# Performance work log

Hardware: AMD Instinct MI355X
Metric: run time of the kernel (lower is better)

The kernel has to match this reference:

```python
import jax, jax.numpy as jnp
import numpy as np

H, C = 5, 128          # heads, hidden_channels
NUM_GRAPHS = 500
N_NODES, N_EDGES = 20000, 320000


def gat_layer(x, edge_attr, src, dst, W, We, a_src, a_dst, a_edge, b):
    """PyG GATConv with edge_dim, add_self_loops=True, fill_value='mean', concat heads."""
    N = x.shape[0]
    ed = edge_attr.dtype
    # self-loop edge_attr = scatter-mean of incoming edge_attr per target node
    deg = jax.ops.segment_sum(jnp.ones((dst.shape[0],), ed), dst, num_segments=N)
    loop_attr = jax.ops.segment_sum(edge_attr, dst, num_segments=N) / jnp.maximum(deg, 1.0)[:, None]
    loop = jnp.arange(N, dtype=src.dtype)
    s = jnp.concatenate([src, loop])
    d = jnp.concatenate([dst, loop])
    ea = jnp.concatenate([edge_attr, loop_attr], axis=0)
    h = (x @ W).reshape(N, H, C)            # [N,H,C]
    e = (ea @ We).reshape(-1, H, C)         # [E2,H,C]
    a_l = (h * a_src).sum(-1)               # [N,H]
    a_r = (h * a_dst).sum(-1)               # [N,H]
    a_e = (e * a_edge).sum(-1)              # [E2,H]
    alpha = jax.nn.leaky_relu(a_l[s] + a_r[d] + a_e, 0.2)
    # segment softmax over destination neighborhoods
    amax = jax.ops.segment_max(alpha, d, num_segments=N)
    ex = jnp.exp(alpha - amax[d])
    denom = jax.ops.segment_sum(ex, d, num_segments=N)
    att = ex / (denom[d] + 1e-16)           # [E2,H]
    msg = h[s] * att[..., None]             # [E2,H,C]
    out = jax.ops.segment_sum(msg, d, num_segments=N).reshape(N, H * C)
    return out + b


def setup_inputs() -> dict:
    key = jax.random.key(0)
    ks = jax.random.split(key, 24)
    p = lambda k, sh: (jax.random.normal(k, sh, dtype=jnp.float32) * 0.05)
    inp = {
        "x": jax.random.normal(ks[0], (N_NODES, 43), dtype=jnp.float32),
        "edge_attr": jax.random.normal(ks[1], (N_EDGES, 10), dtype=jnp.float32),
        "W1": p(ks[2], (43, H * C)),   "We1": p(ks[3], (10, H * C)),
        "asrc1": p(ks[4], (H, C)), "adst1": p(ks[5], (H, C)), "aedge1": p(ks[6], (H, C)),
        "b1": jnp.zeros((H * C,), jnp.float32),
        "W2": p(ks[7], (H * C, H * C)), "We2": p(ks[8], (10, H * C)),
        "asrc2": p(ks[9], (H, C)), "adst2": p(ks[10], (H, C)), "aedge2": p(ks[11], (H, C)),
        "b2": jnp.zeros((H * C,), jnp.float32),
        "W3": p(ks[12], (H * C, H * C)), "We3": p(ks[13], (10, H * C)),
        "asrc3": p(ks[14], (H, C)), "adst3": p(ks[15], (H, C)), "aedge3": p(ks[16], (H, C)),
        "b3": jnp.zeros((H * C,), jnp.float32),
        "Wlin": p(ks[17], (H * C, 1)), "blin": jnp.zeros((1,), jnp.float32),
        "edge_index": jax.random.randint(ks[18], (2, N_EDGES), 0, N_NODES, dtype=jnp.int32),
        "batch": jnp.sort(jax.random.randint(ks[19], (N_NODES,), 0, NUM_GRAPHS, dtype=jnp.int32)),
    }
    return inp


def reference(x, edge_attr, W1, We1, asrc1, adst1, aedge1, b1,
              W2, We2, asrc2, adst2, aedge2, b2,
              W3, We3, asrc3, adst3, aedge3, b3,
              Wlin, blin, edge_index, batch):
    src, dst = edge_index[0], edge_index[1]
    h = jax.nn.relu(gat_layer(x, edge_attr, src, dst, W1, We1, asrc1, adst1, aedge1, b1))
    h = jax.nn.relu(gat_layer(h, edge_attr, src, dst, W2, We2, asrc2, adst2, aedge2, b2))
    h = gat_layer(h, edge_attr, src, dst, W3, We3, asrc3, adst3, aedge3, b3)
    # global mean pool over graphs
    cnt = jax.ops.segment_sum(jnp.ones((h.shape[0],), h.dtype), batch, num_segments=NUM_GRAPHS)
    pooled = jax.ops.segment_sum(h, batch, num_segments=NUM_GRAPHS) / jnp.maximum(cnt, 1.0)[:, None]
    return (pooled @ Wlin + blin).squeeze(-1)   # [NUM_GRAPHS]
```

## Files before the change

### kernel.cpp

```cpp
#include <hip/hip_runtime.h>

#define N_NODESC 20000
#define N_EDGESC 320000
#define HC 640
#define NGRAPH 500

typedef unsigned short u16;
typedef unsigned int u32;
typedef __attribute__((ext_vector_type(8))) short bf16x8;
typedef __attribute__((ext_vector_type(4))) float f32x4;

__device__ __forceinline__ float wred_sum(float v){
  #pragma unroll
  for(int o=32;o;o>>=1) v += __shfl_xor(v,o,64);
  return v;
}
__device__ __forceinline__ float lrelu(float x){ return x>0.f? x:0.2f*x; }

__device__ __forceinline__ u16 f2bf(float f){
  u32 u=__float_as_uint(f);
  u32 r=u+0x7FFFu+((u>>16)&1u);
  return (u16)(r>>16);
}
__device__ __forceinline__ float bf2f(u16 s){ return __uint_as_float(((u32)s)<<16); }
__device__ __forceinline__ float bflo(u32 w){ return __uint_as_float(w<<16); }
__device__ __forceinline__ float bfhi(u32 w){ return __uint_as_float(w&0xFFFF0000u); }

__device__ __forceinline__ void gload16(const void* g, void* l){
  __builtin_amdgcn_global_load_lds((const __attribute__((address_space(1))) void*)g,
                                   (__attribute__((address_space(3))) void*)l, 16, 0, 0);
}

__device__ __forceinline__ size_t fidx(int r, int k, int KB){
  return ((size_t)(r>>4)*KB + (k>>5))*512 + (((k>>3)&3)*16 + (r&15))*8 + (k&7);
}


__global__ void k_count(const int* __restrict__ dst, int* __restrict__ cnt){
  int i=blockIdx.x*blockDim.x+threadIdx.x;
  if(i>=N_EDGESC) return;
  atomicAdd(&cnt[dst[i]],1);
}

__global__ void k_scan(const int* __restrict__ cnt, int* __restrict__ rptr, int* __restrict__ pos){
  __shared__ int ps[1024];
  int t=threadIdx.x;
  const int CH=20;
  int beg=t*CH, end=min(beg+CH, N_NODESC);
  int s=0;
  for(int i=beg;i<end;i++) s+=cnt[i];
  ps[t]=s; __syncthreads();
  for(int off=1;off<1024;off<<=1){
    int v=(t>=off)? ps[t-off]:0;
    __syncthreads();
    ps[t]+=v;
    __syncthreads();
  }
  int base=ps[t]-s;
  for(int i=beg;i<end;i++){ rptr[i]=base; pos[i]=base; base+=cnt[i]; }
}

__global__ void k_scatter(const int* __restrict__ dst, int* __restrict__ pos,
                          int* __restrict__ eidx, int* __restrict__ dstC){
  int i=blockIdx.x*blockDim.x+threadIdx.x;
  if(i>=N_EDGESC) return;
  int d=dst[i];
  int j=atomicAdd(&pos[d],1);
  eidx[j]=i;
  dstC[j]=d;
}

__global__ void k_csr_edges(const int* __restrict__ eidx, const int* __restrict__ src,
                            const float* __restrict__ eattr,
                            int* __restrict__ srcE, float* __restrict__ eattrC){
  int j=blockIdx.x*blockDim.x+threadIdx.x;
  if(j>=N_EDGESC) return;
  int e=eidx[j];
  srcE[j]=src[e];
  const float* ep=&eattr[(size_t)e*10];
  float* op=&eattrC[(size_t)j*10];
  #pragma unroll
  for(int k=0;k<10;k++) op[k]=ep[k];
}

__global__ __launch_bounds__(256) void k_loop_attr(const float* __restrict__ eattrC,
    const int* __restrict__ rptr, const int* __restrict__ cnt,
    float* __restrict__ lattr){
  int tid=threadIdx.x, lane=tid&63;
  int n=blockIdx.x*4+(tid>>6);
  if(n>=N_NODESC) return;
  int beg=rptr[n], deg=cnt[n];
  float s[10]={0,0,0,0,0,0,0,0,0,0};
  for(int off=lane; off<deg; off+=64){
    const float* ep=&eattrC[(size_t)(beg+off)*10];
    #pragma unroll
    for(int k=0;k<10;k++) s[k]+=ep[k];
  }
  float inv=1.f/fmaxf((float)deg,1.f);
  #pragma unroll
  for(int k=0;k<10;k++){
    float tot=wred_sum(s[k]);
    if(lane==0) lattr[(size_t)n*10+k]=tot*inv;
  }
}


__global__ void k_padx(const float* __restrict__ x, float* __restrict__ xp){
  int idx=blockIdx.x*blockDim.x+threadIdx.x;
  if(idx>=N_NODESC*64) return;
  int n=idx>>6, kk=idx&63;
  xp[idx] = kk<43 ? x[n*43+kk] : 0.f;
}

__global__ void k_conv_w3(const float* __restrict__ W0, const float* __restrict__ W1,
                          const float* __restrict__ W2,
                          u16* __restrict__ hi, u16* __restrict__ lo){
  const int R0=HC*64, R1=R0+HC*HC;
  const int TOT=R1+HC*HC;
  int idx=blockIdx.x*blockDim.x+threadIdx.x;
  if(idx>=TOT) return;
  const float* W; int local, KP, KL, base;
  if(idx<R0){ W=W0; local=idx; KP=64; KL=43; base=0; }
  else if(idx<R1){ W=W1; local=idx-R0; KP=HC; KL=HC; base=R0; }
  else { W=W2; local=idx-R1; KP=HC; KL=HC; base=R1; }
  int n=local/KP, kk=local-n*KP;
  float v = kk<KL ? W[(size_t)kk*HC+n] : 0.f;
  u16 h=f2bf(v);
  size_t off=(size_t)base + fidx(n,kk,KP>>5);
  hi[off]=h;
  lo[off]=f2bf(v-bf2f(h));
}


__global__ void k_ve3(const float* __restrict__ We0, const float* __restrict__ ae0,
                      const float* __restrict__ We1, const float* __restrict__ ae1,
                      const float* __restrict__ We2, const float* __restrict__ ae2,
                      float* __restrict__ ve3){
  int t=threadIdx.x;
  if(t>=150) return;
  int L=t/50, r=t-50*L, k=r/5, h=r%5;
  const float* We = (L==0)?We0:(L==1)?We1:We2;
  const float* ae = (L==0)?ae0:(L==1)?ae1:ae2;
  float s=0.f;
  for(int c=0;c<128;c++) s += We[k*HC + h*128 + c]*ae[h*128+c];
  ve3[t]=s;
}

__global__ void k_vs0(const float* __restrict__ W0, const float* __restrict__ asrc,
                      const float* __restrict__ adst,
                      float* __restrict__ VS, float* __restrict__ VD){
  int t=threadIdx.x;
  if(t>=320) return;
  int k=t/5, h=t%5;
  float sv=0.f, dv=0.f;
  if(k<43){
    for(int c=0;c<128;c++){
      float wv=W0[(size_t)k*HC + h*128 + c];
      sv+=wv*asrc[h*128+c];
      dv+=wv*adst[h*128+c];
    }
  }
  VS[t]=sv; VD[t]=dv;
}

__global__ __launch_bounds__(256) void k_alar0(const float* __restrict__ x,
    const float* __restrict__ VS, const float* __restrict__ VD,
    float* __restrict__ al, float* __restrict__ ar){
  __shared__ float vs[320], vd[320];
  if(threadIdx.x<320){ vs[threadIdx.x]=VS[threadIdx.x]; vd[threadIdx.x]=VD[threadIdx.x]; }
  __syncthreads();
  int idx=blockIdx.x*blockDim.x+threadIdx.x;
  if(idx>=N_NODESC*5) return;
  int n=idx/5, h=idx-5*n;
  float sa=0.f, sd=0.f;
  const float* xr=&x[(size_t)n*43];
  for(int k=0;k<43;k++){
    float xv=xr[k];
    sa+=xv*vs[k*5+h];
    sd+=xv*vd[k*5+h];
  }
  al[idx]=sa; ar[idx]=sd;
}

__global__ void k_cb(const float* __restrict__ bias, const float* __restrict__ wlin,
                     float* __restrict__ cb){
  int lane=threadIdx.x;
  float s=0.f;
  for(int c=lane;c<HC;c+=64) s+=bias[c]*wlin[c];
  s=wred_sum(s);
  if(lane==0) cb[0]=s;
}

__global__ __launch_bounds__(256) void k_edge_terms3(const float* __restrict__ eattrC,
    const float* __restrict__ lattr, const float* __restrict__ ve3,
    float* __restrict__ aeC3, float* __restrict__ ael3){
  __shared__ float ves[150];
  if(threadIdx.x<150) ves[threadIdx.x]=ve3[threadIdx.x];
  __syncthreads();
  const int NEDGET=N_EDGESC+N_NODESC*5;
  int idx=blockIdx.x*blockDim.x+threadIdx.x;
  if(idx>=3*NEDGET) return;
  int L=idx/NEDGET, r=idx-L*NEDGET;
  const float* vl=&ves[L*50];
  if(r<N_EDGESC){
    float ev[10];
    const float* ep=&eattrC[(size_t)r*10];
    #pragma unroll
    for(int k=0;k<10;k++) ev[k]=ep[k];
    #pragma unroll
    for(int hh=0;hh<5;hh++){
      float s=0.f;
      #pragma unroll
      for(int k=0;k<10;k++) s+=ev[k]*vl[k*5+hh];
      aeC3[(size_t)L*N_EDGESC*5 + (size_t)r*5+hh]=s;
    }
  }else{
    int t=r-N_EDGESC;
    int n=t/5, h=t-5*n;
    float s=0.f;
    #pragma unroll
    for(int k=0;k<10;k++) s+=lattr[(size_t)n*10+k]*vl[k*5+h];
    ael3[(size_t)L*N_NODESC*5 + t]=s;
  }
}

__global__ void k_edgew(const int* __restrict__ srcE, const int* __restrict__ dstC,
                        const float* __restrict__ al, const float* __restrict__ ar,
                        const float* __restrict__ aeC, float* __restrict__ wE){
  int j=blockIdx.x*blockDim.x+threadIdx.x;
  if(j>=N_EDGESC) return;
  int s=srcE[j], d=dstC[j];
  const float* av=&aeC[(size_t)j*5];
  float* wp=&wE[(size_t)j*5];
  #pragma unroll
  for(int h=0;h<5;h++)
    wp[h]=__expf(lrelu(al[s*5+h]+ar[d*5+h]+av[h]));
}


__global__ __launch_bounds__(256) void k_aggx(const float* __restrict__ xp,
    const int* __restrict__ srcE, const int* __restrict__ rptr, const int* __restrict__ cnt,
    const float* __restrict__ al, const float* __restrict__ ar, const float* __restrict__ ael,
    const float* __restrict__ wE,
    u16* __restrict__ aggx, float* __restrict__ den0){
  const size_t HSZ=(size_t)N_NODESC*64;
  int tid=threadIdx.x, lane=tid&63;
  int n=blockIdx.x*4+(tid>>6);
  if(n>=N_NODESC) return;
  float den[5], acc[5];
  #pragma unroll
  for(int h=0;h<5;h++)
    den[h]=__expf(lrelu(al[n*5+h]+ar[n*5+h]+ael[n*5+h]));
  float xn=xp[(size_t)n*64+lane];
  #pragma unroll
  for(int h=0;h<5;h++) acc[h]=den[h]*xn;
  int beg=rptr[n], end=beg+cnt[n];
  int j=beg;
  for(; j+7<end; j+=8){
    int sj[8]; float xv[8];
    #pragma unroll
    for(int u=0;u<8;u++) sj[u]=srcE[j+u];
    #pragma unroll
    for(int u=0;u<8;u++) xv[u]=xp[(size_t)sj[u]*64+lane];
    #pragma unroll
    for(int u=0;u<8;u++){
      const float* wp=&wE[(size_t)(j+u)*5];
      #pragma unroll
      for(int h=0;h<5;h++){
        float w=wp[h];
        den[h]+=w;
        acc[h]+=w*xv[u];
      }
    }
  }
  for(; j<end; j++){
    int sj=srcE[j];
    float xv=xp[(size_t)sj*64+lane];
    const float* wp=&wE[(size_t)j*5];
    #pragma unroll
    for(int h=0;h<5;h++){
      float w=wp[h];
      den[h]+=w;
      acc[h]+=w*xv;
    }
  }
  size_t fo=fidx(n,lane,2);
  #pragma unroll
  for(int h=0;h<5;h++) aggx[(size_t)h*HSZ+fo]=f2bf(acc[h]);
  if(lane<5) den0[(size_t)n*5+lane]=den[lane];
}

__global__ __launch_bounds__(256,3) void k_gemm_l0b(
    const u16* __restrict__ AGX,
    const u16* __restrict__ Bhi, const u16* __restrict__ Blo,
    const float* __restrict__ den0, const float* __restrict__ bias,
    u16* __restrict__ A1, int M, int nblk){
  const size_t HSZ=(size_t)N_NODESC*64;
  __shared__ u16 lds[2*3*4096];
  int tid=threadIdx.x;
  int lane=tid&63;
  int w=tid>>6;
  int l15=lane&15, lg=lane>>4;
  int orig=blockIdx.x;
  int q=nblk>>3, r=nblk&7;
  int xcd=orig&7, off=orig>>3;
  int wg=(xcd<r? xcd*(q+1) : r*(q+1)+(xcd-r)*q)+off;
  int by=wg/5, bx=wg-5*by;
  int row0=by*128, col0=bx*128;
  int wr=w>>1, wc=w&1;
  const u16* A=AGX+(size_t)bx*HSZ;

  f32x4 zero = {0.f,0.f,0.f,0.f};
  f32x4 acc[4][4];
  #pragma unroll
  for(int i=0;i<4;i++)
    #pragma unroll
    for(int j=0;j<4;j++) acc[i][j]=zero;

  auto stage=[&](int b, int k0){
    u16* base = lds + b*3*4096;
    int kb=k0>>5;
    #pragma unroll
    for(int c=0;c<2;c++){
      int sb=w+4*c;
      size_t af=((size_t)((row0>>4)+sb)*2 + kb)*512 + lane*8;
      size_t bf=((size_t)((col0>>4)+sb)*2 + kb)*512 + lane*8;
      gload16(A+af, base + sb*512);
      gload16(Bhi+bf, base+4096 + sb*512);
      gload16(Blo+bf, base+8192 + sb*512);
    }
  };

  stage(0,0);
  __syncthreads();
  int cur=0;
  for(int t=0;t<2;t++){
    if(t==0) stage(1,32);
    u16* cb = lds + cur*3*4096;
    bf16x8 ah[4], bh[4], bl[4];
    #pragma unroll
    for(int i=0;i<4;i++){
      ah[i]=*(const bf16x8*)&cb[(wr*4+i)*512 + lane*8];
      bh[i]=*(const bf16x8*)&cb[4096+(wc*4+i)*512 + lane*8];
      bl[i]=*(const bf16x8*)&cb[8192+(wc*4+i)*512 + lane*8];
    }
    #pragma unroll
    for(int i=0;i<4;i++)
      #pragma unroll
      for(int j=0;j<4;j++){
        acc[i][j]=__builtin_amdgcn_mfma_f32_16x16x32_bf16(ah[i],bh[j],acc[i][j],0,0,0);
        acc[i][j]=__builtin_amdgcn_mfma_f32_16x16x32_bf16(ah[i],bl[j],acc[i][j],0,0,0);
      }
    __syncthreads();
    cur^=1;
  }

  #pragma unroll
  for(int i=0;i<4;i++){
    #pragma unroll
    for(int j=0;j<4;j++){
      int col=col0+wc*64+j*16+l15;
      float bv=bias[col];
      #pragma unroll
      for(int rr=0;rr<4;rr++){
        int row=row0+wr*64+i*16+lg*4+rr;
        if(row<M){
          float dv=den0[(size_t)row*5+bx];
          float v=acc[i][j][rr]/(dv+1e-16f)+bv;
          v=fmaxf(v,0.f);
          A1[fidx(row,col,20)]=f2bf(v);
        }
      }
    }
  }
}


template<bool HB, bool QOUT>
__global__ __launch_bounds__(256,6) void k_gemm64(
    const u16* __restrict__ A,
    const u16* __restrict__ B,
    const float* __restrict__ asrc, const float* __restrict__ adst,
    const float* __restrict__ wlin,
    u16* __restrict__ hb, float* __restrict__ al, float* __restrict__ ar,
    float* __restrict__ qn,
    int M, int KP, int nblk){
  __shared__ u16 lds[2*6144];
  int tid=threadIdx.x;
  int lane=tid&63;
  int w=tid>>6;
  int l15=lane&15, lg=lane>>4;
  int orig=blockIdx.x;
  int q=nblk>>3, r=nblk&7;
  int xcd=orig&7, off=orig>>3;
  int wg=(xcd<r? xcd*(q+1) : r*(q+1)+(xcd-r)*q)+off;
  int by=wg/5, bx=wg-5*by;
  int row0=by*64, col0=bx*128;
  int KB=KP>>5;

  f32x4 zero = {0.f,0.f,0.f,0.f};
  f32x4 acc[4][2];
  #pragma unroll
  for(int i=0;i<4;i++){ acc[i][0]=zero; acc[i][1]=zero; }

  auto stage=[&](int b, int k0){
    u16* base = lds + b*6144;
    int kb=k0>>5;
    size_t af=((size_t)((row0>>4)+w)*KB + kb)*512 + lane*8;
    gload16(A+af, base + w*512);
    #pragma unroll
    for(int c=0;c<2;c++){
      int sb=w+4*c;
      size_t bf=((size_t)((col0>>4)+sb)*KB + kb)*512 + lane*8;
      gload16(B+bf, base+2048 + sb*512);
    }
  };

  int nt=KP/32;
  stage(0,0);
  __syncthreads();
  int cur=0;
  for(int t=0;t<nt;t++){
    if(t+1<nt) stage(cur^1,(t+1)*32);
    u16* cb = lds + cur*6144;
    bf16x8 ah[4], bh[2];
    #pragma unroll
    for(int i=0;i<4;i++) ah[i]=*(const bf16x8*)&cb[i*512 + lane*8];
    #pragma unroll
    for(int j=0;j<2;j++) bh[j]=*(const bf16x8*)&cb[2048+(w*2+j)*512 + lane*8];
    #pragma unroll
    for(int i=0;i<4;i++){
      acc[i][0]=__builtin_amdgcn_mfma_f32_16x16x32_bf16(ah[i],bh[0],acc[i][0],0,0,0);
      acc[i][1]=__builtin_amdgcn_mfma_f32_16x16x32_bf16(ah[i],bh[1],acc[i][1],0,0,0);
    }
    __syncthreads();
    cur^=1;
  }

  float asv[2], adv[2], wlv[2];
  #pragma unroll
  for(int j=0;j<2;j++){
    int c=col0+w*32+j*16+l15;
    asv[j]=asrc[c]; adv[j]=adst[c];
    if(QOUT) wlv[j]=wlin[c];
  }
  if(HB){
    #pragma unroll
    for(int i=0;i<4;i++){
      #pragma unroll
      for(int j=0;j<2;j++){
        #pragma unroll
        for(int rr=0;rr<4;rr++){
          int row=row0+i*16+lg*4+rr;
          if(row<M)
            hb[(size_t)row*HC + ((w&1)*32+j*16+l15)*10 + bx*2+(w>>1)]=f2bf(acc[i][j][rr]);
        }
      }
    }
  }
  float* redAl=(float*)lds;
  float* redAr=redAl+256;
  float* redQ =redAr+256;
  #pragma unroll
  for(int i=0;i<4;i++){
    #pragma unroll
    for(int rr=0;rr<4;rr++){
      float sa=0.f, sd=0.f, sq=0.f;
      #pragma unroll
      for(int j=0;j<2;j++){
        sa+=acc[i][j][rr]*asv[j];
        sd+=acc[i][j][rr]*adv[j];
        if(QOUT) sq+=acc[i][j][rr]*wlv[j];
      }
      #pragma unroll
      for(int o=1;o<16;o<<=1){
        sa+=__shfl_xor(sa,o,64); sd+=__shfl_xor(sd,o,64);
        if(QOUT) sq+=__shfl_xor(sq,o,64);
      }
      if(l15==0){
        int lr=i*16+lg*4+rr;
        redAl[lr*4+w]=sa; redAr[lr*4+w]=sd;
        if(QOUT) redQ[lr*4+w]=sq;
      }
    }
  }
  __syncthreads();
  if(tid<64){
    int row=row0+tid;
    if(row<M){
      al[(size_t)row*5+bx]=redAl[tid*4]+redAl[tid*4+1]+redAl[tid*4+2]+redAl[tid*4+3];
      ar[(size_t)row*5+bx]=redAr[tid*4]+redAr[tid*4+1]+redAr[tid*4+2]+redAr[tid*4+3];
      if(QOUT) qn[(size_t)row*5+bx]=redQ[tid*4]+redQ[tid*4+1]+redQ[tid*4+2]+redQ[tid*4+3];
    }
  }
}

__global__ __launch_bounds__(256) void k_agg(const u16* __restrict__ hb, const int* __restrict__ srcE,
    const int* __restrict__ rptr, const int* __restrict__ cnt,
    const float* __restrict__ al, const float* __restrict__ ar, const float* __restrict__ ael,
    const float* __restrict__ wE, const float* __restrict__ bias,
    u16* __restrict__ ohi){
  int tid=threadIdx.x, lane=tid&63;
  int n=blockIdx.x*4+(tid>>6);
  if(n>=N_NODESC) return;
  float den[5], acc[10];
  #pragma unroll
  for(int h=0;h<5;h++)
    den[h]=__expf(lrelu(al[n*5+h]+ar[n*5+h]+ael[n*5+h]));
  {
    const u32* sp=(const u32*)(hb+(size_t)n*HC+lane*10);
    #pragma unroll
    for(int j2=0;j2<5;j2++){
      u32 wv=sp[j2];
      acc[2*j2]  =den[j2]*bflo(wv);
      acc[2*j2+1]=den[j2]*bfhi(wv);
    }
  }
  int beg=rptr[n], end=beg+cnt[n];
  int j=beg;
  for(; j+3<end; j+=4){
    int sj[4];
    #pragma unroll
    for(int u=0;u<4;u++) sj[u]=srcE[j+u];
    float w[4][5];
    #pragma unroll
    for(int u=0;u<4;u++){
      const float* wp=&wE[(size_t)(j+u)*5];
      #pragma unroll
      for(int h=0;h<5;h++) w[u][h]=wp[h];
    }
    u32 wv[4][5];
    #pragma unroll
    for(int u=0;u<4;u++){
      const u32* hr=(const u32*)(hb+(size_t)sj[u]*HC+lane*10);
      #pragma unroll
      for(int j2=0;j2<5;j2++) wv[u][j2]=hr[j2];
    }
    #pragma unroll
    for(int u=0;u<4;u++){
      #pragma unroll
      for(int j2=0;j2<5;j2++){
        den[j2]+=w[u][j2];
        acc[2*j2]  +=w[u][j2]*bflo(wv[u][j2]);
        acc[2*j2+1]+=w[u][j2]*bfhi(wv[u][j2]);
      }
    }
  }
  for(; j<end; j++){
    int sj=srcE[j];
    const float* wp=&wE[(size_t)j*5];
    float w[5];
    #pragma unroll
    for(int h=0;h<5;h++){ w[h]=wp[h]; den[h]+=w[h]; }
    const u32* hr=(const u32*)(hb+(size_t)sj*HC+lane*10);
    #pragma unroll
    for(int j2=0;j2<5;j2++){
      u32 wv=hr[j2];
      acc[2*j2]  +=w[j2]*bflo(wv);
      acc[2*j2+1]+=w[j2]*bfhi(wv);
    }
  }
  #pragma unroll
  for(int k=0;k<10;k++){
    int ccol=lane+64*k;
    float vv=acc[k]/(den[k>>1]+1e-16f)+bias[ccol];
    vv=fmaxf(vv,0.f);
    ohi[fidx(n,ccol,20)]=f2bf(vv);
  }
}

__global__ __launch_bounds__(256) void k_agg_last(const float* __restrict__ qn,
    const int* __restrict__ srcE, const int* __restrict__ rptr, const int* __restrict__ cnt,
    const float* __restrict__ al, const float* __restrict__ ar, const float* __restrict__ ael,
    const float* __restrict__ aeC, const float* __restrict__ cb,
    float* __restrict__ pnode){
  int tid=threadIdx.x;
  int sub=tid&15;
  int n=blockIdx.x*16+(tid>>4);
  if(n>=N_NODESC) return;
  float arn[5], den[5], qs[5];
  #pragma unroll
  for(int h=0;h<5;h++) arn[h]=ar[n*5+h];
  #pragma unroll
  for(int h=0;h<5;h++){ den[h]=0.f; qs[h]=0.f; }
  if(sub==0){
    #pragma unroll
    for(int h=0;h<5;h++){
      float pp=__expf(lrelu(al[n*5+h]+arn[h]+ael[n*5+h]));
      den[h]=pp; qs[h]=pp*qn[(size_t)n*5+h];
    }
  }
  int beg=rptr[n], deg=cnt[n];
  for(int off=sub; off<deg; off+=16){
    int j=beg+off;
    int s=srcE[j];
    const float* av=&aeC[(size_t)j*5];
    const float* qv=&qn[(size_t)s*5];
    #pragma unroll
    for(int h=0;h<5;h++){
      float pp=__expf(lrelu(al[s*5+h]+arn[h]+av[h]));
      den[h]+=pp; qs[h]+=pp*qv[h];
    }
  }
  #pragma unroll
  for(int h=0;h<5;h++){
    #pragma unroll
    for(int o=1;o<16;o<<=1){
      den[h]+=__shfl_xor(den[h],o,16);
      qs[h]+=__shfl_xor(qs[h],o,16);
    }
  }
  if(sub==0){
    float s=0.f;
    #pragma unroll
    for(int h=0;h<5;h++) s+=qs[h]/(den[h]+1e-16f);
    pnode[n]=s+cb[0];
  }
}

__global__ __launch_bounds__(256) void k_graphout(const float* __restrict__ pnode,
    const int* __restrict__ batch, const float* __restrict__ blin,
    float* __restrict__ out){
  int tid=threadIdx.x, lane=tid&63;
  int g=blockIdx.x*4+(tid>>6);
  if(g>=NGRAPH) return;
  auto lb=[&](int val){
    int lo=0, hi=N_NODESC;
    while(lo<hi){ int mid=(lo+hi)>>1; if(batch[mid]<val) lo=mid+1; else hi=mid; }
    return lo;
  };
  int s0=lb(g), s1=lb(g+1);
  float s=0.f;
  for(int i=s0+lane;i<s1;i+=64) s+=pnode[i];
  s=wred_sum(s);
  if(lane==0) out[g]=s/fmaxf((float)(s1-s0),1.f)+blin[0];
}


extern "C" void kernel_launch(void* const* d_in, const int* in_sizes, int n_in,
                              void* d_out, int out_size, void* d_ws, size_t ws_size,
                              hipStream_t stream){
  const float* x     = (const float*)d_in[0];
  const float* eattr = (const float*)d_in[1];
  const float* W[3]    ={(const float*)d_in[2],(const float*)d_in[8],(const float*)d_in[14]};
  const float* We[3]   ={(const float*)d_in[3],(const float*)d_in[9],(const float*)d_in[15]};
  const float* asrc[3] ={(const float*)d_in[4],(const float*)d_in[10],(const float*)d_in[16]};
  const float* adst[3] ={(const float*)d_in[5],(const float*)d_in[11],(const float*)d_in[17]};
  const float* aedge[3]={(const float*)d_in[6],(const float*)d_in[12],(const float*)d_in[18]};
  const float* bias[3] ={(const float*)d_in[7],(const float*)d_in[13],(const float*)d_in[19]};
  const float* Wlin  = (const float*)d_in[20];
  const float* blin  = (const float*)d_in[21];
  const int* eind    = (const int*)d_in[22];
  const int* srcp    = eind;
  const int* dstp    = eind + N_EDGESC;
  const int* batch   = (const int*)d_in[23];
  float* out = (float*)d_out;

  char* ws=(char*)d_ws;
  size_t o=0;
  auto alloc=[&](size_t bytes)->void*{ void* p=ws+o; o=(o+bytes+255)&~(size_t)255; return p; };
  u16* hb   =(u16*)alloc((size_t)N_NODESC*HC*2);
  u16* Ahi =(u16*)alloc((size_t)N_NODESC*HC*2);
  float* xp =(float*)alloc((size_t)N_NODESC*64*4);
  u16* aggx=(u16*)alloc((size_t)5*N_NODESC*64*2);
  const int WB0=0, WB1=HC*64, WB2=WB1+HC*HC;
  u16* Bthi3=(u16*)alloc((size_t)(WB2+HC*HC)*2);
  u16* Btlo3=(u16*)alloc((size_t)(WB2+HC*HC)*2);
  float* al   =(float*)alloc((size_t)N_NODESC*5*4);
  float* ar   =(float*)alloc((size_t)N_NODESC*5*4);
  float* qn   =(float*)alloc((size_t)N_NODESC*5*4);
  float* den0 =(float*)alloc((size_t)N_NODESC*5*4);
  float* ael3 =(float*)alloc((size_t)3*N_NODESC*5*4);
  float* aeC3 =(float*)alloc((size_t)3*N_EDGESC*5*4);
  float* wE   =(float*)alloc((size_t)N_EDGESC*5*4);
  float* lattr=(float*)alloc((size_t)N_NODESC*10*4);
  float* eattrC=(float*)alloc((size_t)N_EDGESC*10*4);
  float* ve3  =(float*)alloc(256*4);
  float* VS0  =(float*)alloc(320*4);
  float* VD0  =(float*)alloc(320*4);
  float* cbv  =(float*)alloc(64*4);
  float* pnode=(float*)alloc((size_t)N_NODESC*4);
  int* cntI   =(int*)alloc((size_t)N_NODESC*4);
  int* rptr   =(int*)alloc((size_t)N_NODESC*4);
  int* pos    =(int*)alloc((size_t)N_NODESC*4);
  int* eidx   =(int*)alloc((size_t)N_EDGESC*4);
  int* srcE   =(int*)alloc((size_t)N_EDGESC*4);
  int* dstC   =(int*)alloc((size_t)N_EDGESC*4);

  hipMemsetAsync(cntI,0,(size_t)N_NODESC*4,stream);

  k_count<<<(N_EDGESC+255)/256,256,0,stream>>>(dstp,cntI);
  k_scan<<<1,1024,0,stream>>>(cntI,rptr,pos);
  k_scatter<<<(N_EDGESC+255)/256,256,0,stream>>>(dstp,pos,eidx,dstC);
  k_csr_edges<<<(N_EDGESC+255)/256,256,0,stream>>>(eidx,srcp,eattr,srcE,eattrC);
  k_loop_attr<<<(N_NODESC+3)/4,256,0,stream>>>(eattrC,rptr,cntI,lattr);
  k_padx<<<(N_NODESC*64+255)/256,256,0,stream>>>(x,xp);
  k_ve3<<<1,256,0,stream>>>(We[0],aedge[0],We[1],aedge[1],We[2],aedge[2],ve3);
  k_vs0<<<1,320,0,stream>>>(W[0],asrc[0],adst[0],VS0,VD0);
  k_cb<<<1,64,0,stream>>>(bias[2],Wlin,cbv);
  {
    int tot=WB2+HC*HC;
    k_conv_w3<<<(tot+255)/256,256,0,stream>>>(W[0],W[1],W[2],Bthi3,Btlo3);
  }
  {
    const int NEDGET=N_EDGESC+N_NODESC*5;
    k_edge_terms3<<<(3*NEDGET+255)/256,256,0,stream>>>(eattrC,lattr,ve3,aeC3,ael3);
  }
  k_alar0<<<(N_NODESC*5+255)/256,256,0,stream>>>(x,VS0,VD0,al,ar);

  const int NBLK0=5*((N_NODESC+127)/128);
  const int NBLK64=5*((N_NODESC+63)/64);

  k_edgew<<<(N_EDGESC+255)/256,256,0,stream>>>(srcE,dstC,al,ar,aeC3,wE);
  k_aggx<<<(N_NODESC+3)/4,256,0,stream>>>(xp,srcE,rptr,cntI,al,ar,ael3,wE,aggx,den0);
  k_gemm_l0b<<<NBLK0,256,0,stream>>>(aggx,Bthi3+WB0,Btlo3+WB0,den0,bias[0],Ahi,N_NODESC,NBLK0);

  {
    const float* aeL = aeC3 + (size_t)1*N_EDGESC*5;
    const float* aelL= ael3 + (size_t)1*N_NODESC*5;
    k_gemm64<true,false><<<NBLK64,256,0,stream>>>(Ahi,Bthi3+WB1,
        asrc[1],adst[1],Wlin,hb,al,ar,qn,N_NODESC,HC,NBLK64);
    k_edgew<<<(N_EDGESC+255)/256,256,0,stream>>>(srcE,dstC,al,ar,aeL,wE);
    k_agg<<<(N_NODESC+3)/4,256,0,stream>>>(hb,srcE,rptr,cntI,al,ar,aelL,wE,bias[1],Ahi);
  }
  {
    const float* aeL = aeC3 + (size_t)2*N_EDGESC*5;
    const float* aelL= ael3 + (size_t)2*N_NODESC*5;
    k_gemm64<false,true><<<NBLK64,256,0,stream>>>(Ahi,Bthi3+WB2,
        asrc[2],adst[2],Wlin,hb,al,ar,qn,N_NODESC,HC,NBLK64);
    k_agg_last<<<(N_NODESC+15)/16,256,0,stream>>>(qn,srcE,rptr,cntI,al,ar,aelL,aeC3+(size_t)2*N_EDGESC*5,cbv,pnode);
  }
  k_graphout<<<(NGRAPH+3)/4,256,0,stream>>>(pnode,batch,blin,out);
}
```

Baseline: 393.9 us.

## Triple-buffer gemm64 LDS pipeline and fuse CSR edge gather into scatter

The 64-row GEMM moves from double to triple LDS buffering. It uses explicit vmcnt waits and raw s_barrier so two K-tiles of global loads stay in flight while the current tile is computed, with the occupancy hint lowered from 6 to 4 to fit the larger LDS. The CSR build also writes src and edge attributes directly at the scattered position, removing the eidx array and the separate k_csr_edges launch. The risks are lower occupancy and the correctness of the hand-counted vmcnt values, which assume exactly three outstanding loads per stage.

```diff
diff --git a/kernel.cpp b/kernel.cpp
--- a/kernel.cpp
+++ b/kernel.cpp
@@ -60,24 +60,17 @@
   for(int i=beg;i<end;i++){ rptr[i]=base; pos[i]=base; base+=cnt[i]; }
 }
 
-__global__ void k_scatter(const int* __restrict__ dst, int* __restrict__ pos,
-                          int* __restrict__ eidx, int* __restrict__ dstC){
+__global__ void k_scatter(const int* __restrict__ dst, const int* __restrict__ src,
+                          const float* __restrict__ eattr, int* __restrict__ pos,
+                          int* __restrict__ srcE, int* __restrict__ dstC,
+                          float* __restrict__ eattrC){
   int i=blockIdx.x*blockDim.x+threadIdx.x;
   if(i>=N_EDGESC) return;
   int d=dst[i];
   int j=atomicAdd(&pos[d],1);
-  eidx[j]=i;
   dstC[j]=d;
-}
-
-__global__ void k_csr_edges(const int* __restrict__ eidx, const int* __restrict__ src,
-                            const float* __restrict__ eattr,
-                            int* __restrict__ srcE, float* __restrict__ eattrC){
-  int j=blockIdx.x*blockDim.x+threadIdx.x;
-  if(j>=N_EDGESC) return;
-  int e=eidx[j];
-  srcE[j]=src[e];
-  const float* ep=&eattr[(size_t)e*10];
+  srcE[j]=src[i];
+  const float* ep=&eattr[(size_t)i*10];
   float* op=&eattrC[(size_t)j*10];
   #pragma unroll
   for(int k=0;k<10;k++) op[k]=ep[k];
@@ -377,7 +370,7 @@
 
 
 template<bool HB, bool QOUT>
-__global__ __launch_bounds__(256,6) void k_gemm64(
+__global__ __launch_bounds__(256,4) void k_gemm64(
     const u16* __restrict__ A,
     const u16* __restrict__ B,
     const float* __restrict__ asrc, const float* __restrict__ adst,
@@ -385,7 +378,7 @@
     u16* __restrict__ hb, float* __restrict__ al, float* __restrict__ ar,
     float* __restrict__ qn,
     int M, int KP, int nblk){
-  __shared__ u16 lds[2*6144];
+  __shared__ u16 lds[3*6144];
   int tid=threadIdx.x;
   int lane=tid&63;
   int w=tid>>6;
@@ -418,11 +411,16 @@
 
   int nt=KP/32;
   stage(0,0);
-  __syncthreads();
-  int cur=0;
+  if(nt>1) stage(1,32);
   for(int t=0;t<nt;t++){
-    if(t+1<nt) stage(cur^1,(t+1)*32);
-    u16* cb = lds + cur*6144;
+    int nb=t+2;
+    if(nb<nt) stage(nb%3, nb*32);
+    if(nb<nt)      { asm volatile("s_waitcnt vmcnt(6)" ::: "memory"); }
+    else if(t+1<nt){ asm volatile("s_waitcnt vmcnt(3)" ::: "memory"); }
+    else           { asm volatile("s_waitcnt vmcnt(0)" ::: "memory"); }
+    __builtin_amdgcn_sched_barrier(0);
+    __builtin_amdgcn_s_barrier();
+    u16* cb = lds + (t%3)*6144;
     bf16x8 ah[4], bh[2];
     #pragma unroll
     for(int i=0;i<4;i++) ah[i]=*(const bf16x8*)&cb[i*512 + lane*8];
@@ -433,9 +431,9 @@
       acc[i][0]=__builtin_amdgcn_mfma_f32_16x16x32_bf16(ah[i],bh[0],acc[i][0],0,0,0);
       acc[i][1]=__builtin_amdgcn_mfma_f32_16x16x32_bf16(ah[i],bh[1],acc[i][1],0,0,0);
     }
-    __syncthreads();
-    cur^=1;
-  }
+    __builtin_amdgcn_s_barrier();
+  }
+  __syncthreads();
 
   float asv[2], adv[2], wlv[2];
   #pragma unroll
@@ -683,7 +681,6 @@
   int* cntI   =(int*)alloc((size_t)N_NODESC*4);
   int* rptr   =(int*)alloc((size_t)N_NODESC*4);
   int* pos    =(int*)alloc((size_t)N_NODESC*4);
-  int* eidx   =(int*)alloc((size_t)N_EDGESC*4);
   int* srcE   =(int*)alloc((size_t)N_EDGESC*4);
   int* dstC   =(int*)alloc((size_t)N_EDGESC*4);
 
@@ -691,8 +688,7 @@
 
   k_count<<<(N_EDGESC+255)/256,256,0,stream>>>(dstp,cntI);
   k_scan<<<1,1024,0,stream>>>(cntI,rptr,pos);
-  k_scatter<<<(N_EDGESC+255)/256,256,0,stream>>>(dstp,pos,eidx,dstC);
-  k_csr_edges<<<(N_EDGESC+255)/256,256,0,stream>>>(eidx,srcp,eattr,srcE,eattrC);
+  k_scatter<<<(N_EDGESC+255)/256,256,0,stream>>>(dstp,srcp,eattr,pos,srcE,dstC,eattrC);
   k_loop_attr<<<(N_NODESC+3)/4,256,0,stream>>>(eattrC,rptr,cntI,lattr);
   k_padx<<<(N_NODESC*64+255)/256,256,0,stream>>>(x,xp);
   k_ve3<<<1,256,0,stream>>>(We[0],aedge[0],We[1],aedge[1],We[2],aedge[2],ve3);
@@ -724,7 +720,6 @@
     k_agg<<<(N_NODESC+3)/4,256,0,stream>>>(hb,srcE,rptr,cntI,al,ar,aelL,wE,bias[1],Ahi);
   }
   {
-    const float* aeL = aeC3 + (size_t)2*N_EDGESC*5;
     const float* aelL= ael3 + (size_t)2*N_NODESC*5;
     k_gemm64<false,true><<<NBLK64,256,0,stream>>>(Ahi,Bthi3+WB2,
         asrc[2],adst[2],Wlin,hb,al,ar,qn,N_NODESC,HC,NBLK64);
```

Measured after the change: 382.6 us. -2.9%, faster.
